# Optimization experiments

Hardware: AMD Instinct MI355X
Metric: run time of the kernel (lower is better)

## Reference

```python
import jax, jax.numpy as jnp
import numpy as np

B, S, D, H = 8, 2048, 1024, 128  # batch, seq (== CONTEXT_WINDOW), embed dim, headspace


def setup_inputs() -> dict:
    key = jax.random.key(0)
    ks = jax.random.split(key, 7)
    scale = 1.0 / np.sqrt(D)
    return {
        "x": jax.random.normal(ks[0], (B, S, D), dtype=jnp.float32),
        "Wq": jax.random.normal(ks[1], (D, H), dtype=jnp.float32) * scale,
        "bq": jax.random.normal(ks[2], (H,), dtype=jnp.float32) * 0.01,
        "Wk": jax.random.normal(ks[3], (D, H), dtype=jnp.float32) * scale,
        "bk": jax.random.normal(ks[4], (H,), dtype=jnp.float32) * 0.01,
        "Wv": jax.random.normal(ks[5], (D, H), dtype=jnp.float32) * scale,
        "bv": jax.random.normal(ks[6], (H,), dtype=jnp.float32) * 0.01,
    }


def reference(x, Wq, bq, Wk, bk, Wv, bv):
    # x: [B, S, D]
    embedlen = x.shape[-1]
    q = x @ Wq + bq  # [B, S, H]
    k = x @ Wk + bk  # [B, S, H]
    v = x @ Wv + bv  # [B, S, H]
    # NOTE: original code MULTIPLIES by sqrt(embedlen) (embedlen = full embed dim) --
    # faithful reproduction of the source, not the standard 1/sqrt(head_dim).
    scale = jnp.sqrt(jnp.asarray(embedlen, dtype=x.dtype))
    scores = jnp.einsum("bsh,bth->bst", q, k) * scale  # [B, S, S]
    seqlen = x.shape[1]
    causal = jnp.tril(jnp.ones((seqlen, seqlen), dtype=bool))
    scores = jnp.where(causal, scores, -jnp.inf)
    attn = jax.nn.softmax(scores, axis=-1)
    return jnp.einsum("bst,bth->bsh", attn, v)  # [B, S, H]
```

## Files before the change

### kernel.cpp

```cpp
#include <hip/hip_runtime.h>
#include <math.h>

#define SEQ 2048
#define DIM 1024
#define HD  128
#define NB  8
#define M_TOT (NB * SEQ)

typedef __attribute__((ext_vector_type(8))) short   short8;
typedef __attribute__((ext_vector_type(4))) float   floatx4;

__device__ __forceinline__ unsigned short f2bf(float f) {
    unsigned u = __builtin_bit_cast(unsigned, f);
    u += 0x7FFFu + ((u >> 16) & 1u);
    return (unsigned short)(u >> 16);
}
__device__ __forceinline__ float bf2f(unsigned short h) {
    unsigned u = ((unsigned)h) << 16;
    return __builtin_bit_cast(float, u);
}
__device__ __forceinline__ void async16(const void* g, void* l) {
    __builtin_amdgcn_global_load_lds(
        (const __attribute__((address_space(1))) unsigned int*)g,
        (__attribute__((address_space(3))) unsigned int*)l, 16, 0, 0);
}

#define MFMA16(a, b, c) __builtin_amdgcn_mfma_f32_16x16x32_bf16((a), (b), (c), 0, 0, 0)

__global__ __launch_bounds__(256) void wt_prep(
    const float* __restrict__ Wq, const float* __restrict__ Wk, const float* __restrict__ Wv,
    unsigned short* __restrict__ Wth, unsigned short* __restrict__ Wtl)
{
    int idx = blockIdx.x * 256 + threadIdx.x;
    int k   = idx & 1023;
    int n   = (idx >> 10) & 127;
    int mat = idx >> 17;
    const float* W = (mat == 0) ? Wq : (mat == 1) ? Wk : Wv;
    float v = W[k * HD + n];
    unsigned short hi = f2bf(v);
    Wth[idx] = hi;
    Wtl[idx] = f2bf(v - bf2f(hi));
}

__global__ __launch_bounds__(512, 4) void qkv_fused(
    const float* __restrict__ x,
    const unsigned short* __restrict__ Wth, const unsigned short* __restrict__ Wtl,
    const float* __restrict__ bq, const float* __restrict__ bk, const float* __restrict__ bv,
    unsigned short* __restrict__ Qh, unsigned short* __restrict__ Ql,
    unsigned short* __restrict__ Kh, unsigned short* __restrict__ Kl,
    unsigned short* __restrict__ Vt)
{
    __shared__ short lds[56 * 512];

    const int t    = threadIdx.x;
    const int lane = t & 63;
    const int w    = t >> 6;
    const int lrow = lane & 15;
    const int quad = lane >> 4;

    const int R0 = blockIdx.x * 32;

    auto stageB = [&](int k0, int qb) {
        #pragma unroll
        for (int i = 0; i < 3; ++i) {
            int bf  = w * 3 + i;
            int mat = bf >> 3, nf = bf & 7;
            const unsigned short* src = Wth + (size_t)mat * (HD * DIM)
                + (size_t)(nf * 16 + lrow) * DIM + k0 + quad * 8;
            async16(src, &lds[(8 + qb * 24 + bf) * 512 + lane * 8]);
        }
    };

    const int arow = t >> 4;
    const int akk  = (t & 15) * 2;
    auto xload = [&](int k0) -> float2 {
        return *(const float2*)&x[(size_t)(R0 + arow) * DIM + k0 + akk];
    };
    auto stageA = [&](float2 xv, int qb) {
        unsigned short h0 = f2bf(xv.x), h1 = f2bf(xv.y);
        unsigned short l0 = f2bf(xv.x - bf2f(h0)), l1 = f2bf(xv.y - bf2f(h1));
        int mi = arow >> 4, lr = arow & 15, qd = akk >> 3, el = akk & 7;
        int base = (qb * 4 + mi * 2) * 512 + (qd * 16 + lr) * 8 + el;
        short2 hv; hv.x = (short)h0; hv.y = (short)h1;
        short2 lv; lv.x = (short)l0; lv.y = (short)l1;
        *(short2*)&lds[base]       = hv;
        *(short2*)&lds[base + 512] = lv;
    };

    const unsigned short* bloQ = Wtl + (size_t)(w * 16 + lrow) * DIM + quad * 8;
    const unsigned short* bloK = bloQ + (size_t)(HD * DIM);

    floatx4 acc[2][3];
    const floatx4 zf = {0.f, 0.f, 0.f, 0.f};
    #pragma unroll
    for (int mi = 0; mi < 2; ++mi)
        #pragma unroll
        for (int c = 0; c < 3; ++c) acc[mi][c] = zf;

    float2 xn = xload(0);
    stageA(xn, 0);
    stageB(0, 0);
    xn = xload(32);

    for (int it = 0; it < 32; ++it) {
        __syncthreads();
        const int k0 = it * 32;
        const int q  = it & 1;

        short8 blq = *(const short8*)(bloQ + k0);
        short8 blk = *(const short8*)(bloK + k0);

        if (it < 31) {
            stageB(k0 + 32, q ^ 1);
            stageA(xn, q ^ 1);
        }
        if (it < 30) xn = xload(k0 + 64);

        short8 a[2][2];
        #pragma unroll
        for (int mi = 0; mi < 2; ++mi)
            #pragma unroll
            for (int p = 0; p < 2; ++p)
                a[mi][p] = *(short8*)&lds[(q * 4 + mi * 2 + p) * 512 + lane * 8];

        short8 bhq = *(short8*)&lds[(8 + q * 24 +  0 + w) * 512 + lane * 8];
        short8 bhk = *(short8*)&lds[(8 + q * 24 +  8 + w) * 512 + lane * 8];
        short8 bhv = *(short8*)&lds[(8 + q * 24 + 16 + w) * 512 + lane * 8];

        #pragma unroll
        for (int mi = 0; mi < 2; ++mi) {
            acc[mi][0] = MFMA16(a[mi][0], bhq, acc[mi][0]);
            acc[mi][1] = MFMA16(a[mi][0], bhk, acc[mi][1]);
            acc[mi][2] = MFMA16(a[mi][0], bhv, acc[mi][2]);
            acc[mi][0] = MFMA16(a[mi][1], bhq, acc[mi][0]);
            acc[mi][1] = MFMA16(a[mi][1], bhk, acc[mi][1]);
            acc[mi][0] = MFMA16(a[mi][0], blq, acc[mi][0]);
            acc[mi][1] = MFMA16(a[mi][0], blk, acc[mi][1]);
        }
    }

    const int col = w * 16 + lrow;
    const float bqv = bq[col], bkv = bk[col], bvv = bv[col];
    #pragma unroll
    for (int mi = 0; mi < 2; ++mi) {
        #pragma unroll
        for (int reg = 0; reg < 4; ++reg) {
            int gm = R0 + mi * 16 + quad * 4 + reg;
            float vq = (acc[mi][0][reg] + bqv) * 32.0f;
            unsigned short h = f2bf(vq);
            Qh[(size_t)gm * HD + col] = h;
            Ql[(size_t)gm * HD + col] = f2bf(vq - bf2f(h));
            float vk = acc[mi][1][reg] + bkv;
            h = f2bf(vk);
            Kh[(size_t)gm * HD + col] = h;
            Kl[(size_t)gm * HD + col] = f2bf(vk - bf2f(h));
            float vv = acc[mi][2][reg] + bvv;
            int b = gm >> 11, s = gm & 2047;
            Vt[((size_t)b * HD + col) * SEQ + s] = f2bf(vv);
        }
    }
}

__global__ __launch_bounds__(256) void flash_attn(
    const unsigned short* __restrict__ Qh, const unsigned short* __restrict__ Ql,
    const unsigned short* __restrict__ Kh, const unsigned short* __restrict__ Kl,
    const unsigned short* __restrict__ Vt, float* __restrict__ out,
    float* __restrict__ Opart, float* __restrict__ ML, int split)
{
    __shared__ short lds[52 * 512];

    const int t    = threadIdx.x;
    const int lane = t & 63;
    const int w    = t >> 6;
    const int lrow = lane & 15;
    const int quad = lane >> 4;

    const int idx = blockIdx.x;
    const int b   = idx & 7;
    const int h   = split ? ((idx >> 3) & 1) : 0;
    const int s   = split ? (63 - (idx >> 4)) : (63 - (idx >> 3));
    const int T   = (s + 2) >> 1;
    const int Th  = (T + 1) >> 1;
    const int t0  = split ? (h ? Th : 0) : 0;
    const int t1  = split ? (h ? T : Th) : T;

    if (split && t0 >= t1) {
        float* op = Opart + (size_t)idx * 4096;
        for (int i = t; i < 4096; i += 256) op[i] = 0.0f;
        if (t < 32) { ML[(idx * 32 + t) * 2] = -1e30f; ML[(idx * 32 + t) * 2 + 1] = 0.0f; }
        return;
    }

    const int mh = w & 1;
    const int kh = w >> 1;
    const int R  = s * 32 + mh * 16;

    const size_t kbase = (size_t)b * SEQ * HD;
    const size_t vbase = (size_t)b * HD * SEQ;

    short8 qf[4][2];
    #pragma unroll
    for (int kc = 0; kc < 4; ++kc) {
        size_t off = kbase + (size_t)(R + lrow) * HD + kc * 32 + quad * 8;
        qf[kc][0] = *(const short8*)(Qh + off);
        qf[kc][1] = *(const short8*)(Ql + off);
    }

    const floatx4 zf = {0.f, 0.f, 0.f, 0.f};
    floatx4 accO[8];
    #pragma unroll
    for (int i = 0; i < 8; ++i) accO[i] = zf;
    float m_[4] = {-1e30f, -1e30f, -1e30f, -1e30f};
    float l_[4] = {0.f, 0.f, 0.f, 0.f};

    for (int it = t0; it < t1; ++it) {
        const int j0 = it * 64;
        __syncthreads();
        #pragma unroll
        for (int i = 0; i < 12; ++i) {
            int id = w * 12 + i;
            const unsigned short* src;
            if (id < 32) {
                int nt = id >> 3, kc = (id >> 1) & 3, p = id & 1;
                src = (p ? Kl : Kh) + kbase
                    + (size_t)(j0 + nt * 16 + lrow) * HD + kc * 32 + quad * 8;
            } else {
                int v = id - 32, df = v >> 1, kc = v & 1;
                src = Vt + vbase + (size_t)(df * 16 + lrow) * SEQ
                    + j0 + kc * 32 + quad * 8;
            }
            async16(src, &lds[id * 512 + lane * 8]);
        }
        __syncthreads();

        floatx4 S[2] = {zf, zf};
        #pragma unroll
        for (int ntl = 0; ntl < 2; ++ntl) {
            int nt = kh * 2 + ntl;
            #pragma unroll
            for (int kc = 0; kc < 4; ++kc) {
                short8 khf = *(short8*)&lds[(nt * 8 + kc * 2 + 0) * 512 + lane * 8];
                short8 klf = *(short8*)&lds[(nt * 8 + kc * 2 + 1) * 512 + lane * 8];
                S[ntl] = MFMA16(qf[kc][0], khf, S[ntl]);
                S[ntl] = MFMA16(qf[kc][0], klf, S[ntl]);
                S[ntl] = MFMA16(qf[kc][1], khf, S[ntl]);
            }
        }
        if (j0 + kh * 32 + 31 > R) {
            #pragma unroll
            for (int ntl = 0; ntl < 2; ++ntl) {
                int key = j0 + (kh * 2 + ntl) * 16 + lrow;
                #pragma unroll
                for (int reg = 0; reg < 4; ++reg) {
                    if (key > R + quad * 4 + reg) S[ntl][reg] = -INFINITY;
                }
            }
        }
        float alpha[4];
        #pragma unroll
        for (int reg = 0; reg < 4; ++reg) {
            float mx = fmaxf(S[0][reg], S[1][reg]);
            #pragma unroll
            for (int hh = 1; hh < 16; hh <<= 1) mx = fmaxf(mx, __shfl_xor(mx, hh));
            float mnew = fmaxf(fmaxf(m_[reg], mx), -1e30f);
            alpha[reg] = __expf(m_[reg] - mnew);
            m_[reg] = mnew;
            float p0 = __expf(S[0][reg] - mnew);
            float p1 = __expf(S[1][reg] - mnew);
            S[0][reg] = p0; S[1][reg] = p1;
            float ls = p0 + p1;
            #pragma unroll
            for (int hh = 1; hh < 16; hh <<= 1) ls += __shfl_xor(ls, hh);
            l_[reg] = l_[reg] * alpha[reg] + ls;
        }
        #pragma unroll
        for (int i = 0; i < 8; ++i)
            #pragma unroll
            for (int reg = 0; reg < 4; ++reg) accO[i][reg] *= alpha[reg];

        #pragma unroll
        for (int ntl = 0; ntl < 2; ++ntl) {
            #pragma unroll
            for (int reg = 0; reg < 4; ++reg) {
                int kloc = ntl * 16 + lrow;
                int jj = kloc & 7, q2 = (kloc >> 3) & 3;
                int lane2 = (quad * 4 + reg) + (q2 << 4);
                lds[(48 + w) * 512 + lane2 * 8 + jj] = (short)f2bf(S[ntl][reg]);
            }
        }
        short8 pf = *(short8*)&lds[(48 + w) * 512 + lane * 8];
        #pragma unroll
        for (int df = 0; df < 8; ++df) {
            short8 vf = *(short8*)&lds[(32 + df * 2 + kh) * 512 + lane * 8];
            accO[df] = MFMA16(pf, vf, accO[df]);
        }
    }

    __syncthreads();
    float* fl   = (float*)lds;
    float* Obuf = fl;
    float* mlb  = fl + 4096;
    if (lrow == 0) {
        #pragma unroll
        for (int reg = 0; reg < 4; ++reg) {
            int row = quad * 4 + reg;
            mlb[((kh * 2 + mh) * 16 + row) * 2 + 0] = m_[reg];
            mlb[((kh * 2 + mh) * 16 + row) * 2 + 1] = l_[reg];
        }
    }
    __syncthreads();
    float myw[4], Mrow[4], Drow[4];
    #pragma unroll
    for (int reg = 0; reg < 4; ++reg) {
        int row = quad * 4 + reg;
        float mo  = mlb[(((1 - kh) * 2 + mh) * 16 + row) * 2 + 0];
        float lo_ = mlb[(((1 - kh) * 2 + mh) * 16 + row) * 2 + 1];
        float M = fmaxf(m_[reg], mo);
        float d = l_[reg] * __expf(m_[reg] - M) + lo_ * __expf(mo - M);
        Mrow[reg] = M; Drow[reg] = d;
        myw[reg] = split ? __expf(m_[reg] - M) : (__expf(m_[reg] - M) / d);
    }
    if (kh == 0) {
        #pragma unroll
        for (int df = 0; df < 8; ++df)
            #pragma unroll
            for (int reg = 0; reg < 4; ++reg)
                Obuf[(mh * 16 + quad * 4 + reg) * 128 + df * 16 + lrow] =
                    accO[df][reg] * myw[reg];
    }
    __syncthreads();
    if (kh == 1) {
        if (split) {
            float* op = Opart + (size_t)idx * 4096;
            #pragma unroll
            for (int df = 0; df < 8; ++df) {
                #pragma unroll
                for (int reg = 0; reg < 4; ++reg) {
                    int row = mh * 16 + quad * 4 + reg;
                    op[row * 128 + df * 16 + lrow] =
                        Obuf[row * 128 + df * 16 + lrow] + accO[df][reg] * myw[reg];
                }
            }
            if (lrow == 0) {
                #pragma unroll
                for (int reg = 0; reg < 4; ++reg) {
                    int row = mh * 16 + quad * 4 + reg;
                    ML[(idx * 32 + row) * 2 + 0] = Mrow[reg];
                    ML[(idx * 32 + row) * 2 + 1] = Drow[reg];
                }
            }
        } else {
            #pragma unroll
            for (int df = 0; df < 8; ++df) {
                #pragma unroll
                for (int reg = 0; reg < 4; ++reg) {
                    float v = Obuf[(mh * 16 + quad * 4 + reg) * 128 + df * 16 + lrow]
                            + accO[df][reg] * myw[reg];
                    size_t o = ((size_t)(b * SEQ + R + quad * 4 + reg)) * HD + df * 16 + lrow;
                    out[o] = v;
                }
            }
        }
    }
}

__global__ __launch_bounds__(256) void splitk_merge(
    const float* __restrict__ Opart, const float* __restrict__ ML,
    float* __restrict__ out)
{
    int tid = blockIdx.x * 256 + threadIdx.x;
    int row = tid >> 5, c4 = tid & 31;
    int b = row >> 11, r = row & 2047, s = r >> 5, rr = r & 31;
    int i0 = ((63 - s) << 4) + b;
    int i1 = i0 + 8;
    float m0 = ML[(i0 * 32 + rr) * 2], l0 = ML[(i0 * 32 + rr) * 2 + 1];
    float m1 = ML[(i1 * 32 + rr) * 2], l1 = ML[(i1 * 32 + rr) * 2 + 1];
    float M  = fmaxf(m0, m1);
    float w0 = __expf(m0 - M), w1 = __expf(m1 - M);
    float inv = 1.0f / (w0 * l0 + w1 * l1);
    float4 a  = *(const float4*)&Opart[((size_t)i0 * 32 + rr) * 128 + c4 * 4];
    float4 bb = *(const float4*)&Opart[((size_t)i1 * 32 + rr) * 128 + c4 * 4];
    float4 o;
    o.x = (w0 * a.x + w1 * bb.x) * inv;
    o.y = (w0 * a.y + w1 * bb.y) * inv;
    o.z = (w0 * a.z + w1 * bb.z) * inv;
    o.w = (w0 * a.w + w1 * bb.w) * inv;
    *(float4*)&out[(size_t)row * 128 + c4 * 4] = o;
}

extern "C" void kernel_launch(void* const* d_in, const int* in_sizes, int n_in,
                              void* d_out, int out_size, void* d_ws, size_t ws_size,
                              hipStream_t stream) {
    const float* x  = (const float*)d_in[0];
    const float* Wq = (const float*)d_in[1];
    const float* bq = (const float*)d_in[2];
    const float* Wk = (const float*)d_in[3];
    const float* bk = (const float*)d_in[4];
    const float* Wv = (const float*)d_in[5];
    const float* bv = (const float*)d_in[6];
    float* out = (float*)d_out;

    unsigned short* Qh  = (unsigned short*)d_ws;
    unsigned short* Ql  = Qh  + (size_t)M_TOT * HD;
    unsigned short* Kh  = Ql  + (size_t)M_TOT * HD;
    unsigned short* Kl  = Kh  + (size_t)M_TOT * HD;
    unsigned short* Vt  = Kl  + (size_t)M_TOT * HD;
    unsigned short* Wth = Vt  + (size_t)M_TOT * HD;
    unsigned short* Wtl = Wth + (size_t)3 * HD * DIM;
    float* Opart = (float*)(Wtl + (size_t)3 * HD * DIM);
    float* ML    = Opart + (size_t)1024 * 32 * 128;

    const size_t need = 22544384ULL + 16777216ULL + 262144ULL;
    const int split = (ws_size >= need) ? 1 : 0;

    wt_prep<<<(3 * HD * DIM) / 256, 256, 0, stream>>>(Wq, Wk, Wv, Wth, Wtl);
    qkv_fused<<<512, 512, 0, stream>>>(x, Wth, Wtl, bq, bk, bv, Qh, Ql, Kh, Kl, Vt);
    flash_attn<<<split ? 1024 : 512, 256, 0, stream>>>(Qh, Ql, Kh, Kl, Vt, out, Opart, ML, split);
    if (split) splitk_merge<<<2048, 256, 0, stream>>>(Opart, ML, out);
}
```

Measured before the change: 250.5 us.

## Double QKV projection block to 64 rows and stage low weight halves in LDS

The QKV projection kernel now uses 1024-thread blocks covering 64 rows, with 16 waves split into 2 row halves × 8 column tiles. This doubles reuse of each staged weight tile. The low-order bf16 weight parts for Q and K are now loaded asynchronously into LDS alongside the high parts, instead of being read per-wave from global memory each iteration. This cuts global/L2 weight traffic, at the cost of larger LDS use, fewer blocks, and tighter register limits per thread.

```diff
diff --git a/kernel.cpp b/kernel.cpp
--- a/kernel.cpp
+++ b/kernel.cpp
@@ -42,7 +42,7 @@
     Wtl[idx] = f2bf(v - bf2f(hi));
 }
 
-__global__ __launch_bounds__(512, 4) void qkv_fused(
+__global__ __launch_bounds__(1024, 4) void qkv_fused(
     const float* __restrict__ x,
     const unsigned short* __restrict__ Wth, const unsigned short* __restrict__ Wtl,
     const float* __restrict__ bq, const float* __restrict__ bk, const float* __restrict__ bv,
@@ -50,7 +50,7 @@
     unsigned short* __restrict__ Kh, unsigned short* __restrict__ Kl,
     unsigned short* __restrict__ Vt)
 {
-    __shared__ short lds[56 * 512];
+    __shared__ short lds[96 * 512];
 
     const int t    = threadIdx.x;
     const int lane = t & 63;
@@ -58,16 +58,22 @@
     const int lrow = lane & 15;
     const int quad = lane >> 4;
 
-    const int R0 = blockIdx.x * 32;
+    const int R0 = blockIdx.x * 64;
+    const int mh = w & 1;
+    const int nh = w >> 1;
 
     auto stageB = [&](int k0, int qb) {
         #pragma unroll
         for (int i = 0; i < 3; ++i) {
-            int bf  = w * 3 + i;
-            int mat = bf >> 3, nf = bf & 7;
-            const unsigned short* src = Wth + (size_t)mat * (HD * DIM)
-                + (size_t)(nf * 16 + lrow) * DIM + k0 + quad * 8;
-            async16(src, &lds[(8 + qb * 24 + bf) * 512 + lane * 8]);
+            int f = i * 16 + w;
+            if (f < 40) {
+                int p   = (f >= 24);
+                int ff  = p ? (f - 24) : f;
+                int mat = ff >> 3, nf = ff & 7;
+                const unsigned short* src = (p ? Wtl : Wth) + (size_t)mat * (HD * DIM)
+                    + (size_t)(nf * 16 + lrow) * DIM + k0 + quad * 8;
+                async16(src, &lds[(qb * 48 + 8 + f) * 512 + lane * 8]);
+            }
         }
     };
 
@@ -80,22 +86,19 @@
         unsigned short h0 = f2bf(xv.x), h1 = f2bf(xv.y);
         unsigned short l0 = f2bf(xv.x - bf2f(h0)), l1 = f2bf(xv.y - bf2f(h1));
         int mi = arow >> 4, lr = arow & 15, qd = akk >> 3, el = akk & 7;
-        int base = (qb * 4 + mi * 2) * 512 + (qd * 16 + lr) * 8 + el;
+        int base = (qb * 48 + mi * 2) * 512 + (qd * 16 + lr) * 8 + el;
         short2 hv; hv.x = (short)h0; hv.y = (short)h1;
         short2 lv; lv.x = (short)l0; lv.y = (short)l1;
         *(short2*)&lds[base]       = hv;
         *(short2*)&lds[base + 512] = lv;
     };
 
-    const unsigned short* bloQ = Wtl + (size_t)(w * 16 + lrow) * DIM + quad * 8;
-    const unsigned short* bloK = bloQ + (size_t)(HD * DIM);
-
     floatx4 acc[2][3];
     const floatx4 zf = {0.f, 0.f, 0.f, 0.f};
     #pragma unroll
-    for (int mi = 0; mi < 2; ++mi)
-        #pragma unroll
-        for (int c = 0; c < 3; ++c) acc[mi][c] = zf;
+    for (int mi2 = 0; mi2 < 2; ++mi2)
+        #pragma unroll
+        for (int c = 0; c < 3; ++c) acc[mi2][c] = zf;
 
     float2 xn = xload(0);
     stageA(xn, 0);
@@ -107,9 +110,6 @@
         const int k0 = it * 32;
         const int q  = it & 1;
 
-        short8 blq = *(const short8*)(bloQ + k0);
-        short8 blk = *(const short8*)(bloK + k0);
-
         if (it < 31) {
             stageB(k0 + 32, q ^ 1);
             stageA(xn, q ^ 1);
@@ -118,43 +118,45 @@
 
         short8 a[2][2];
         #pragma unroll
-        for (int mi = 0; mi < 2; ++mi)
+        for (int mi2 = 0; mi2 < 2; ++mi2)
             #pragma unroll
             for (int p = 0; p < 2; ++p)
-                a[mi][p] = *(short8*)&lds[(q * 4 + mi * 2 + p) * 512 + lane * 8];
-
-        short8 bhq = *(short8*)&lds[(8 + q * 24 +  0 + w) * 512 + lane * 8];
-        short8 bhk = *(short8*)&lds[(8 + q * 24 +  8 + w) * 512 + lane * 8];
-        short8 bhv = *(short8*)&lds[(8 + q * 24 + 16 + w) * 512 + lane * 8];
-
-        #pragma unroll
-        for (int mi = 0; mi < 2; ++mi) {
-            acc[mi][0] = MFMA16(a[mi][0], bhq, acc[mi][0]);
-            acc[mi][1] = MFMA16(a[mi][0], bhk, acc[mi][1]);
-            acc[mi][2] = MFMA16(a[mi][0], bhv, acc[mi][2]);
-            acc[mi][0] = MFMA16(a[mi][1], bhq, acc[mi][0]);
-            acc[mi][1] = MFMA16(a[mi][1], bhk, acc[mi][1]);
-            acc[mi][0] = MFMA16(a[mi][0], blq, acc[mi][0]);
-            acc[mi][1] = MFMA16(a[mi][0], blk, acc[mi][1]);
-        }
-    }
-
-    const int col = w * 16 + lrow;
+                a[mi2][p] = *(short8*)&lds[(q * 48 + (mh * 2 + mi2) * 2 + p) * 512 + lane * 8];
+
+        short8 bhq = *(short8*)&lds[(q * 48 + 8 +  0 + nh) * 512 + lane * 8];
+        short8 bhk = *(short8*)&lds[(q * 48 + 8 +  8 + nh) * 512 + lane * 8];
+        short8 bhv = *(short8*)&lds[(q * 48 + 8 + 16 + nh) * 512 + lane * 8];
+        short8 blq = *(short8*)&lds[(q * 48 + 8 + 24 + nh) * 512 + lane * 8];
+        short8 blk = *(short8*)&lds[(q * 48 + 8 + 32 + nh) * 512 + lane * 8];
+
+        #pragma unroll
+        for (int mi2 = 0; mi2 < 2; ++mi2) {
+            acc[mi2][0] = MFMA16(a[mi2][0], bhq, acc[mi2][0]);
+            acc[mi2][1] = MFMA16(a[mi2][0], bhk, acc[mi2][1]);
+            acc[mi2][2] = MFMA16(a[mi2][0], bhv, acc[mi2][2]);
+            acc[mi2][0] = MFMA16(a[mi2][1], bhq, acc[mi2][0]);
+            acc[mi2][1] = MFMA16(a[mi2][1], bhk, acc[mi2][1]);
+            acc[mi2][0] = MFMA16(a[mi2][0], blq, acc[mi2][0]);
+            acc[mi2][1] = MFMA16(a[mi2][0], blk, acc[mi2][1]);
+        }
+    }
+
+    const int col = nh * 16 + lrow;
     const float bqv = bq[col], bkv = bk[col], bvv = bv[col];
     #pragma unroll
-    for (int mi = 0; mi < 2; ++mi) {
+    for (int mi2 = 0; mi2 < 2; ++mi2) {
         #pragma unroll
         for (int reg = 0; reg < 4; ++reg) {
-            int gm = R0 + mi * 16 + quad * 4 + reg;
-            float vq = (acc[mi][0][reg] + bqv) * 32.0f;
+            int gm = R0 + (mh * 2 + mi2) * 16 + quad * 4 + reg;
+            float vq = (acc[mi2][0][reg] + bqv) * 32.0f;
             unsigned short h = f2bf(vq);
             Qh[(size_t)gm * HD + col] = h;
             Ql[(size_t)gm * HD + col] = f2bf(vq - bf2f(h));
-            float vk = acc[mi][1][reg] + bkv;
+            float vk = acc[mi2][1][reg] + bkv;
             h = f2bf(vk);
             Kh[(size_t)gm * HD + col] = h;
             Kl[(size_t)gm * HD + col] = f2bf(vk - bf2f(h));
-            float vv = acc[mi][2][reg] + bvv;
+            float vv = acc[mi2][2][reg] + bvv;
             int b = gm >> 11, s = gm & 2047;
             Vt[((size_t)b * HD + col) * SEQ + s] = f2bf(vv);
         }
@@ -414,7 +416,7 @@
     const int split = (ws_size >= need) ? 1 : 0;
 
     wt_prep<<<(3 * HD * DIM) / 256, 256, 0, stream>>>(Wq, Wk, Wv, Wth, Wtl);
-    qkv_fused<<<512, 512, 0, stream>>>(x, Wth, Wtl, bq, bk, bv, Qh, Ql, Kh, Kl, Vt);
+    qkv_fused<<<256, 1024, 0, stream>>>(x, Wth, Wtl, bq, bk, bv, Qh, Ql, Kh, Kl, Vt);
     flash_attn<<<split ? 1024 : 512, 256, 0, stream>>>(Qh, Ql, Kh, Kl, Vt, out, Opart, ML, split);
     if (split) splitk_merge<<<2048, 256, 0, stream>>>(Opart, ML, out);
 }
```

Result: faster. 227.5 us (-9.2%).
